# Optimization experiments

Hardware: AMD Instinct MI355X
Metric: run time of the kernel (lower is better)

Reference implementation:

```python
import jax, jax.numpy as jnp
import numpy as np

B, T, S = 4, 4096, 4096
D_MODEL = 512        # d_query = d_value_in = d_key_in
N_HEADS = 8
D_KEY = 512
D_VALUE = 512
N_OMEGA = 64
EPS = 1e-9
DK_H = D_KEY // N_HEADS      # 64
DV_H = D_VALUE // N_HEADS    # 64


def _glorot(key, shape):
    fan_in, fan_out = shape[-2], shape[-1]
    lim = np.sqrt(6.0 / (fan_in + fan_out))
    return jax.random.uniform(key, shape, jnp.float32, -lim, lim)


def _draw_omega(key, d_feature, n_omega):
    # n_omega == d_feature here -> single orthogonal block scaled by sqrt(d)
    g = jax.random.normal(key, (d_feature, d_feature), jnp.float32)
    q, _ = jnp.linalg.qr(g)
    q = q * jnp.sqrt(jnp.float32(d_feature))
    return q[:n_omega]


def setup_inputs() -> dict:
    key = jax.random.key(0)
    ks = jax.random.split(key, 7)
    return {
        "query": 0.5 * jax.random.normal(ks[0], (B, T, D_MODEL), jnp.float32),
        "value": 0.5 * jax.random.normal(ks[1], (B, S, D_MODEL), jnp.float32),
        "key": 0.5 * jax.random.normal(ks[2], (B, S, D_MODEL), jnp.float32),
        "wq": _glorot(ks[3], (N_HEADS, D_MODEL, DK_H)),
        "wv": _glorot(ks[4], (N_HEADS, D_MODEL, DV_H)),
        "wk": _glorot(ks[5], (N_HEADS, D_MODEL, DK_H)),
        "omega": _draw_omega(ks[6], DK_H, N_OMEGA),
    }


def _phi(x, omega):
    # x: (B,H,T,dk_h) -> (B,H,T,2*n_omega) FAVOR+ positive random features
    square_sum = 0.5 * jnp.sum(x * x, axis=-1, keepdims=True)
    xw = jnp.einsum('bhtk,mk->bhtm', x, omega)
    un = jnp.exp(jnp.concatenate([xw, -xw], axis=-1) - square_sum) + EPS
    return un / jnp.sqrt(jnp.float32(2.0 * N_OMEGA))


def reference(query, value, key, wq, wv, wk, omega):
    q = jnp.einsum('btf,hfk->bhtk', query, wq)   # (B,H,T,dk_h)
    v = jnp.einsum('bsd,hdk->bhsk', value, wv)   # (B,H,S,dv_h)
    k = jnp.einsum('bsf,hfk->bhsk', key, wk)     # (B,H,S,dk_h)
    qp = _phi(q, omega)                          # (B,H,T,2M)
    kp = _phi(k, omega)                          # (B,H,S,2M)
    v1 = jnp.concatenate([v, jnp.ones(v.shape[:-1] + (1,), v.dtype)], axis=-1)
    kv = jnp.einsum('bhsm,bhsd->bhmd', kp, v1)   # (B,H,2M,dv_h+1)
    qkv = jnp.einsum('bhtm,bhmd->bhtd', qp, kv)  # (B,H,T,dv_h+1)
    normalizer = qkv[..., -1:]
    out = qkv[..., :-1] / normalizer
    # faithful to original: plain reshape (B,H,T,dv_h) -> (B,T,D_VALUE), no transpose
    return jnp.reshape(out, (B, T, D_VALUE))
```

## Files before the change

### kernel.cpp

```cpp
#include <hip/hip_runtime.h>

typedef _Float16 half8 __attribute__((ext_vector_type(8)));
typedef _Float16 half4_t __attribute__((ext_vector_type(4)));
typedef short short8 __attribute__((ext_vector_type(8)));
typedef unsigned short u16x4 __attribute__((ext_vector_type(4)));
typedef float f32x4 __attribute__((ext_vector_type(4)));

#define NH 8

__device__ __forceinline__ unsigned short f2bf(float x) {
  union { float f; unsigned u; } v; v.f = x;
  unsigned r = v.u + 0x7FFFu + ((v.u >> 16) & 1u);
  return (unsigned short)(r >> 16);
}

#define DRAIN_BAR()                                  \
  asm volatile("s_waitcnt lgkmcnt(0)" ::: "memory"); \
  __builtin_amdgcn_s_barrier();                      \
  __builtin_amdgcn_sched_barrier(0)

__global__ __launch_bounds__(256) void k0_qk(
    const float* __restrict__ wq, const float* __restrict__ wk,
    const float* __restrict__ omega,
    _Float16* __restrict__ wxq, _Float16* __restrict__ wxk) {
  const int bid = blockIdx.x;
  const int arr = bid >> 7;
  const int h = (bid >> 4) & 7;
  const int ft = (bid >> 1) & 7;
  const int os = bid & 1;
  const int f = threadIdx.x & 63;
  const int w = threadIdx.x >> 6;
  const float* wsrc = (arr ? wk : wq) + ((size_t)h * 512 + ft * 64 + f) * 64;
  float wreg[64];
#pragma unroll
  for (int i = 0; i < 16; ++i) {
    float4 v = *(const float4*)(wsrc + i * 4);
    wreg[i * 4] = v.x; wreg[i * 4 + 1] = v.y; wreg[i * 4 + 2] = v.z; wreg[i * 4 + 3] = v.w;
  }
  _Float16* outp = arr ? wxk : wxq;
  const int k8 = f >> 3, e = f & 7;
#pragma unroll 1
  for (int oo = 0; oo < 8; ++oo) {
    const int o = w * 16 + os * 8 + oo;
    const float* om = omega + o * 64;
    float s = 0.f;
#pragma unroll
    for (int k = 0; k < 64; ++k) s = fmaf(wreg[k], om[k], s);
    outp[((((size_t)h * 8 + ft) * 8 + k8) * 64 + o) * 8 + e] = (_Float16)s;
  }
}

__global__ __launch_bounds__(256) void k0_v(
    const float* __restrict__ wv, _Float16* __restrict__ wvt) {
  int idx = blockIdx.x * 256 + threadIdx.x;
  int h = idx >> 15, o = (idx >> 9) & 63, f = idx & 511;
  float val = wv[((size_t)h * 512 + f) * 64 + o];
  wvt[((((size_t)h * 8 + (f >> 6)) * 8 + ((f >> 3) & 7)) * 64 + o) * 8 + (f & 7)] = (_Float16)val;
}

__global__ __launch_bounds__(512, 1) void fused_kv(
    const float* __restrict__ key, const float* __restrict__ value,
    const _Float16* __restrict__ wxk, const _Float16* __restrict__ wvt,
    float* __restrict__ kvpart) {
  __shared__ __align__(16) _Float16 A[2][128][72];
  __shared__ __align__(16) _Float16 W[2][2][4096];
  __shared__ __align__(16) unsigned short kpT[128][136];
  __shared__ __align__(16) unsigned short vT[64][136];
  const int bid = blockIdx.x;
  const int hp = bid >> 6;
  const int b = (bid >> 4) & 3;
  const int sc = bid & 15;
  const int s0 = sc * 256;
  const int tid = threadIdx.x;
  const int w = tid >> 6;
  const int lane = tid & 63;
  const int g = lane >> 4, c = lane & 15;
  const int hh = w >> 2;
  const int rq = w & 3;
  const int xr = lane >> 4;
  const int xc = (lane & 15) * 4;

  const _Float16* wkb0 = wxk + (size_t)(hp * 2) * 32768;
  const _Float16* wkb1 = wkb0 + 32768;
  const _Float16* wvb0 = wvt + (size_t)(hp * 2) * 32768;
  const _Float16* wvb1 = wvb0 + 32768;

  short8 bones;
#pragma unroll
  for (int i = 0; i < 8; ++i) bones[i] = (c == 0) ? (short)0x3F80 : (short)0;

  f32x4 acc_kv[2][5];
#pragma unroll
  for (int h2 = 0; h2 < 2; ++h2)
#pragma unroll
    for (int j = 0; j < 5; ++j) acc_kv[h2][j] = (f32x4){0.f, 0.f, 0.f, 0.f};

  u16x4 kps[2][4], kms[2][4], vs_[2][4];

  float4 xv[4];
  half8 wr0, wr1;

#pragma unroll 1
  for (int p = 0; p < 4; ++p) {
    const float* xb = ((p & 1) ? value : key) +
                      (size_t)(b * 4096 + s0 + (p >> 1) * 128 + w * 16 + xr) * 512 + xc;
    const _Float16* wb0 = (p & 1) ? wvb0 : wkb0;
    const _Float16* wb1 = (p & 1) ? wvb1 : wkb1;

#pragma unroll
    for (int i = 0; i < 4; ++i) xv[i] = *(const float4*)(xb + i * 2048);
    wr0 = *(const half8*)(wb0 + tid * 8);
    wr1 = *(const half8*)(wb1 + tid * 8);
#pragma unroll
    for (int i = 0; i < 4; ++i) {
      float vv[4] = {xv[i].x, xv[i].y, xv[i].z, xv[i].w};
      half4_t hv;
#pragma unroll
      for (int j2 = 0; j2 < 4; ++j2) hv[j2] = (_Float16)vv[j2];
      *(half4_t*)&A[0][w * 16 + i * 4 + xr][xc] = hv;
    }
    *(half8*)&W[0][0][tid * 8] = wr0;
    *(half8*)&W[0][1][tid * 8] = wr1;
#pragma unroll
    for (int i = 0; i < 4; ++i) xv[i] = *(const float4*)(xb + 64 + i * 2048);
    wr0 = *(const half8*)(wb0 + 4096 + tid * 8);
    wr1 = *(const half8*)(wb1 + 4096 + tid * 8);
    DRAIN_BAR();

    f32x4 accp[2][4];
#pragma unroll
    for (int mf = 0; mf < 2; ++mf)
#pragma unroll
      for (int j = 0; j < 4; ++j) accp[mf][j] = (f32x4){0.f, 0.f, 0.f, 0.f};

#pragma unroll 1
    for (int kc = 0; kc < 8; ++kc) {
      const int cur = kc & 1;
      if (kc < 7) {
        const int nxt = cur ^ 1;
#pragma unroll
        for (int i = 0; i < 4; ++i) {
          float vv[4] = {xv[i].x, xv[i].y, xv[i].z, xv[i].w};
          half4_t hv;
#pragma unroll
          for (int j2 = 0; j2 < 4; ++j2) hv[j2] = (_Float16)vv[j2];
          *(half4_t*)&A[nxt][w * 16 + i * 4 + xr][xc] = hv;
        }
        *(half8*)&W[nxt][0][tid * 8] = wr0;
        *(half8*)&W[nxt][1][tid * 8] = wr1;
        if (kc < 6) {
#pragma unroll
          for (int i = 0; i < 4; ++i)
            xv[i] = *(const float4*)(xb + (kc + 2) * 64 + i * 2048);
          wr0 = *(const half8*)(wb0 + (kc + 2) * 4096 + tid * 8);
          wr1 = *(const half8*)(wb1 + (kc + 2) * 4096 + tid * 8);
        }
      }
#pragma unroll
      for (int ks = 0; ks < 2; ++ks) {
        half8 af0 = *(const half8*)&A[cur][rq * 32 + c][ks * 32 + g * 8];
        half8 af1 = *(const half8*)&A[cur][rq * 32 + 16 + c][ks * 32 + g * 8];
#pragma unroll
        for (int nf = 0; nf < 4; ++nf) {
          half8 wf = *(const half8*)&W[cur][hh][((ks * 4 + g) * 64 + nf * 16 + c) * 8];
          accp[0][nf] = __builtin_amdgcn_mfma_f32_16x16x32_f16(af0, wf, accp[0][nf], 0, 0, 0);
          accp[1][nf] = __builtin_amdgcn_mfma_f32_16x16x32_f16(af1, wf, accp[1][nf], 0, 0, 0);
        }
      }
      DRAIN_BAR();
    }

    if ((p & 1) == 0) {
#pragma unroll
      for (int mf = 0; mf < 2; ++mf) {
        float ss_[4];
#pragma unroll
        for (int j = 0; j < 4; ++j) {
          float s = 0.f;
#pragma unroll
          for (int nf = 0; nf < 4; ++nf) { float q = accp[mf][nf][j]; s = fmaf(q, q, s); }
          s += __shfl_xor(s, 1); s += __shfl_xor(s, 2);
          s += __shfl_xor(s, 4); s += __shfl_xor(s, 8);
          ss_[j] = s * 0.0078125f;
        }
#pragma unroll
        for (int nf = 0; nf < 4; ++nf) {
          u16x4 kp_p, kp_m;
#pragma unroll
          for (int j = 0; j < 4; ++j) {
            float v = accp[mf][nf][j];
            kp_p[j] = f2bf(__expf(v - ss_[j]) + 1e-9f);
            kp_m[j] = f2bf(__expf(-v - ss_[j]) + 1e-9f);
          }
          kps[mf][nf] = kp_p;
          kms[mf][nf] = kp_m;
        }
      }
    } else {
#pragma unroll
      for (int mf = 0; mf < 2; ++mf)
#pragma unroll
        for (int nf = 0; nf < 4; ++nf) {
          u16x4 vv;
#pragma unroll
          for (int j = 0; j < 4; ++j) vv[j] = f2bf(accp[mf][nf][j]);
          vs_[mf][nf] = vv;
        }
#pragma unroll
      for (int h2 = 0; h2 < 2; ++h2) {
        if (hh == h2) {
#pragma unroll
          for (int mf = 0; mf < 2; ++mf)
#pragma unroll
            for (int nf = 0; nf < 4; ++nf) {
              const int m = nf * 16 + c;
              const int sl = rq * 32 + mf * 16 + g * 4;
              *(u16x4*)&kpT[m][sl] = kps[mf][nf];
              *(u16x4*)&kpT[64 + m][sl] = kms[mf][nf];
              *(u16x4*)&vT[m][sl] = vs_[mf][nf];
            }
        }
        DRAIN_BAR();
#pragma unroll
        for (int ks = 0; ks < 4; ++ks) {
          short8 a = *(const short8*)&kpT[w * 16 + c][ks * 32 + g * 8];
#pragma unroll
          for (int nf = 0; nf < 4; ++nf) {
            short8 bb = *(const short8*)&vT[nf * 16 + c][ks * 32 + g * 8];
            acc_kv[h2][nf] = __builtin_amdgcn_mfma_f32_16x16x32_bf16(a, bb, acc_kv[h2][nf], 0, 0, 0);
          }
          acc_kv[h2][4] = __builtin_amdgcn_mfma_f32_16x16x32_bf16(a, bones, acc_kv[h2][4], 0, 0, 0);
        }
        __builtin_amdgcn_s_barrier();
      }
    }
  }

#pragma unroll
  for (int h2 = 0; h2 < 2; ++h2) {
    float* pbase = kvpart + ((size_t)sc * 32 + b * 8 + hp * 2 + h2) * 10240;
#pragma unroll
    for (int nf = 0; nf < 5; ++nf)
#pragma unroll
      for (int j = 0; j < 4; ++j)
        pbase[(w * 16 + g * 4 + j) * 80 + nf * 16 + c] = acc_kv[h2][nf][j];
  }
}

__global__ __launch_bounds__(128) void k3a_denom(
    const float* __restrict__ kvpart, float* __restrict__ invbuf,
    float* __restrict__ lsc) {
  const int bh = blockIdx.x;
  const int m = threadIdx.x;
  const float* base = kvpart + (size_t)bh * 10240 + m * 80 + 64;
  float s = 0.f;
#pragma unroll
  for (int kk = 0; kk < 16; ++kk) s += base[(size_t)kk * 327680];
  invbuf[bh * 128 + m] = 1.0f / s;
  lsc[bh * 128 + m] = __logf(s);
}

__global__ __launch_bounds__(256) void k3b_reduce(
    const float* __restrict__ kvpart, const float* __restrict__ invbuf,
    _Float16* __restrict__ kvnt) {
  const int bh = blockIdx.x;
  const int e0 = blockIdx.y * 1024 + threadIdx.x * 4;
  const int m = e0 / 80;
  const int d0 = e0 - m * 80;
  const float* base = kvpart + (size_t)bh * 10240 + e0;
  f32x4 s = (f32x4){0.f, 0.f, 0.f, 0.f};
#pragma unroll
  for (int kk = 0; kk < 16; ++kk) {
    f32x4 v = *(const f32x4*)(base + (size_t)kk * 327680);
    s += v;
  }
  const float inv = invbuf[bh * 128 + m];
  const int mst = ((m & 63) << 1) | (m >> 6);
  _Float16* outb = kvnt + (size_t)bh * 10240 + mst;
#pragma unroll
  for (int j = 0; j < 4; ++j) {
    const int d = d0 + j;
    float val;
    if (d < 64) val = s[j] * inv;
    else if (d == 64) val = 1.0f;
    else val = 0.f;
    outb[d * 128] = (_Float16)val;
  }
}

__global__ __launch_bounds__(256, 2) void fused_qo(
    const float* __restrict__ query, const _Float16* __restrict__ wxq,
    const _Float16* __restrict__ kvnt, const float* __restrict__ lsc,
    float* __restrict__ out) {
  __shared__ __align__(16) _Float16 A[64][264];
  __shared__ __align__(16) _Float16 W[2][4096];
  __shared__ __align__(16) _Float16 qpT[64][136];
  const int bid = blockIdx.x;
  const int hh2 = bid >> 8;
  const int b = (bid >> 6) & 3;
  const int tt = bid & 63;
  const int t0 = tt * 64;
  const int tid = threadIdx.x;
  const int w = tid >> 6;
  const int lane = tid & 63;
  const int g = lane >> 4, c = lane & 15;
  const int arow = tid >> 2;
  const int ac4 = (tid & 3) * 16;

  const float* xrow = query + (size_t)(b * 4096 + t0 + arow) * 512 + ac4;
  const _Float16* wbase = wxq;

  f32x4 accp[4][4];
#pragma unroll
  for (int h = 0; h < 4; ++h)
#pragma unroll
    for (int j = 0; j < 4; ++j) accp[h][j] = (f32x4){0.f, 0.f, 0.f, 0.f};

  float4 xv[4];
  half8 wr0, wr1;

#pragma unroll
  for (int i = 0; i < 4; ++i) xv[i] = *(const float4*)(xrow + i * 64);

#pragma unroll
  for (int kh = 0; kh < 2; ++kh) {
#pragma unroll
    for (int i = 0; i < 4; ++i) {
      float4 v0 = xv[i];
      half4_t hv;
      hv[0] = (_Float16)v0.x; hv[1] = (_Float16)v0.y;
      hv[2] = (_Float16)v0.z; hv[3] = (_Float16)v0.w;
      *(half4_t*)&A[arow][ac4 + i * 4] = hv;
    }
#pragma unroll
    for (int i = 0; i < 4; ++i) {
      float4 v0 = xv[i];
      half4_t hv;
      hv[0] = (_Float16)v0.x; hv[1] = (_Float16)v0.y;
      hv[2] = (_Float16)v0.z; hv[3] = (_Float16)v0.w;
      *(half4_t*)&A[arow][ac4 + i * 64] = hv;
    }
#pragma unroll
    for (int i = 0; i < 4; ++i) {
#pragma unroll
      for (int q2 = 1; q2 < 4; ++q2) {
        float4 v = *(const float4*)(xrow + kh * 256 + i * 64 + q2 * 4);
        half4_t hv;
        hv[0] = (_Float16)v.x; hv[1] = (_Float16)v.y;
        hv[2] = (_Float16)v.z; hv[3] = (_Float16)v.w;
        *(half4_t*)&A[arow][ac4 + i * 64 + q2 * 4] = hv;
      }
    }
    {
      const _Float16* wsl0 = wbase + ((size_t)(hh2 * 4 + 0) * 8 + kh * 4 + 0) * 4096;
      wr0 = *(const half8*)(wsl0 + tid * 8);
      wr1 = *(const half8*)(wsl0 + 2048 + tid * 8);
      *(half8*)&W[0][tid * 8] = wr0;
      *(half8*)&W[0][2048 + tid * 8] = wr1;
      const _Float16* wsl1 = wbase + ((size_t)(hh2 * 4 + 0) * 8 + kh * 4 + 1) * 4096;
      wr0 = *(const half8*)(wsl1 + tid * 8);
      wr1 = *(const half8*)(wsl1 + 2048 + tid * 8);
    }
    DRAIN_BAR();
    if (kh == 0) {
#pragma unroll
      for (int i = 0; i < 4; ++i) xv[i] = *(const float4*)(xrow + 256 + i * 64);
    }

#pragma unroll
    for (int h = 0; h < 4; ++h) {
#pragma unroll
      for (int kc = 0; kc < 4; ++kc) {
        const int s = h * 4 + kc;
        const int cur = s & 1;
        if (s < 15) {
          *(half8*)&W[cur ^ 1][tid * 8] = wr0;
          *(half8*)&W[cur ^ 1][2048 + tid * 8] = wr1;
        }
        if (s < 14) {
          const int sn = s + 2;
          const _Float16* wsl = wbase +
              ((size_t)(hh2 * 4 + (sn >> 2)) * 8 + kh * 4 + (sn & 3)) * 4096;
          wr0 = *(const half8*)(wsl + tid * 8);
          wr1 = *(const half8*)(wsl + 2048 + tid * 8);
        }
#pragma unroll
        for (int ks = 0; ks < 2; ++ks) {
          half8 a = *(const half8*)&A[w * 16 + c][kc * 64 + ks * 32 + g * 8];
#pragma unroll
          for (int nf = 0; nf < 4; ++nf) {
            half8 wf = *(const half8*)&W[cur][((ks * 4 + g) * 64 + nf * 16 + c) * 8];
            accp[h][nf] = __builtin_amdgcn_mfma_f32_16x16x32_f16(a, wf, accp[h][nf], 0, 0, 0);
          }
        }
        DRAIN_BAR();
      }
    }
  }

#pragma unroll
  for (int h = 0; h < 4; ++h) {
    const int bh = b * NH + hh2 * 4 + h;
    float Lp[4], Lm[4];
#pragma unroll
    for (int nf = 0; nf < 4; ++nf) {
      Lp[nf] = lsc[bh * 128 + nf * 16 + c];
      Lm[nf] = lsc[bh * 128 + 64 + nf * 16 + c];
    }
    float ss_[4], cm_[4];
#pragma unroll
    for (int j = 0; j < 4; ++j) {
      float s = 0.f;
#pragma unroll
      for (int nf = 0; nf < 4; ++nf) { float q = accp[h][nf][j]; s = fmaf(q, q, s); }
      s += __shfl_xor(s, 1); s += __shfl_xor(s, 2);
      s += __shfl_xor(s, 4); s += __shfl_xor(s, 8);
      ss_[j] = s * 0.0078125f;
    }
#pragma unroll
    for (int j = 0; j < 4; ++j) {
      float m0 = -1e30f;
#pragma unroll
      for (int nf = 0; nf < 4; ++nf) {
        float v = accp[h][nf][j];
        m0 = fmaxf(m0, fmaxf(v - ss_[j] + Lp[nf], -v - ss_[j] + Lm[nf]));
        m0 = fmaxf(m0, fmaxf(Lp[nf], Lm[nf]) - 20.723265f);
      }
      m0 = fmaxf(m0, __shfl_xor(m0, 1)); m0 = fmaxf(m0, __shfl_xor(m0, 2));
      m0 = fmaxf(m0, __shfl_xor(m0, 4)); m0 = fmaxf(m0, __shfl_xor(m0, 8));
      cm_[j] = m0;
    }
#pragma unroll
    for (int nf = 0; nf < 4; ++nf) {
      const int m = nf * 16 + c;
#pragma unroll
      for (int j = 0; j < 4; ++j) {
        float v = accp[h][nf][j];
        _Float16 pp = (_Float16)(__expf(v - ss_[j] + Lp[nf] - cm_[j]) +
                                 1e-9f * __expf(Lp[nf] - cm_[j]));
        _Float16 pm = (_Float16)(__expf(-v - ss_[j] + Lm[nf] - cm_[j]) +
                                 1e-9f * __expf(Lm[nf] - cm_[j]));
        union { unsigned u; _Float16 hh_[2]; } pk;
        pk.hh_[0] = pp; pk.hh_[1] = pm;
        *(unsigned*)&qpT[w * 16 + g * 4 + j][2 * m] = pk.u;
      }
    }
    DRAIN_BAR();

    f32x4 acco[5];
#pragma unroll
    for (int j = 0; j < 5; ++j) acco[j] = (f32x4){0.f, 0.f, 0.f, 0.f};
    const _Float16* kvb = kvnt + (size_t)bh * 10240;
#pragma unroll
    for (int ks = 0; ks < 4; ++ks) {
      half8 a = *(const half8*)&qpT[w * 16 + c][ks * 32 + g * 8];
#pragma unroll
      for (int nf = 0; nf < 5; ++nf) {
        half8 bb = *(const half8*)(kvb + (size_t)(nf * 16 + c) * 128 + ks * 32 + g * 8);
        acco[nf] = __builtin_amdgcn_mfma_f32_16x16x32_f16(a, bb, acco[nf], 0, 0, 0);
      }
    }
    const int tb = t0 + w * 16 + g * 4;
#pragma unroll
    for (int j = 0; j < 4; ++j) {
      float nrm = __shfl(acco[4][j], (lane & 48));
      float invn = 1.0f / nrm;
#pragma unroll
      for (int nf = 0; nf < 4; ++nf) {
        out[((size_t)bh * 4096 + tb + j) * 64 + nf * 16 + c] = acco[nf][j] * invn;
      }
    }
    DRAIN_BAR();
  }
}

extern "C" void kernel_launch(void* const* d_in, const int* in_sizes, int n_in,
                              void* d_out, int out_size, void* d_ws, size_t ws_size,
                              hipStream_t stream) {
  const float* query = (const float*)d_in[0];
  const float* value = (const float*)d_in[1];
  const float* key   = (const float*)d_in[2];
  const float* wq    = (const float*)d_in[3];
  const float* wv    = (const float*)d_in[4];
  const float* wk    = (const float*)d_in[5];
  const float* omega = (const float*)d_in[6];
  float* out = (float*)d_out;
  char* ws = (char*)d_ws;

  _Float16* wxq  = (_Float16*)(ws);
  _Float16* wxk  = (_Float16*)(ws + 524288);
  _Float16* wvt  = (_Float16*)(ws + 1048576);
  float* kvpart  = (float*)(ws + 1572864);
  _Float16* kvnt = (_Float16*)(ws + 22544384);
  float* lsc     = (float*)(ws + 23199744);
  float* invbuf  = (float*)(ws + 23216128);

  k0_qk<<<256, 256, 0, stream>>>(wq, wk, omega, wxq, wxk);
  k0_v<<<1024, 256, 0, stream>>>(wv, wvt);
  fused_kv<<<256, 512, 0, stream>>>(key, value, wxk, wvt, kvpart);
  k3a_denom<<<32, 128, 0, stream>>>(kvpart, invbuf, lsc);
  k3b_reduce<<<dim3(32, 10), 256, 0, stream>>>(kvpart, invbuf, kvnt);
  fused_qo<<<512, 256, 0, stream>>>(query, wxq, kvnt, lsc, out);
}
```

Measured before the change: 111.3 us.

## Stream fused_qo weights via direct global-to-LDS loads with 4-deep ring buffer

Rewrites the query projection loop in fused_qo so weight tiles go straight from global memory into a 4-slot LDS ring with global_load_lds, issued three stages ahead and gated by vmcnt waits. The register round-trip disappears and each step now needs only one barrier instead of a drain. The A tile shrinks to 128-wide chunks that are reused as the qp buffer, which lowers LDS usage enough to raise occupancy to 3 blocks per SM. The cost is more barrier stages (4 K-chunks instead of 2) and fragile hand-tuned vmcnt counts.

After: 113.9 us. 1.02x slower.

```diff
diff --git a/kernel.cpp b/kernel.cpp
--- a/kernel.cpp
+++ b/kernel.cpp
@@ -18,6 +18,13 @@
   asm volatile("s_waitcnt lgkmcnt(0)" ::: "memory"); \
   __builtin_amdgcn_s_barrier();                      \
   __builtin_amdgcn_sched_barrier(0)
+
+#define WAITVM(N) asm volatile("s_waitcnt vmcnt(" #N ")" ::: "memory")
+
+#define GLOAD_LDS16(g, l)                                             \
+  __builtin_amdgcn_global_load_lds(                                   \
+      (const __attribute__((address_space(1))) unsigned int*)(g),     \
+      (__attribute__((address_space(3))) unsigned int*)(l), 16, 0, 0)
 
 __global__ __launch_bounds__(256) void k0_qk(
     const float* __restrict__ wq, const float* __restrict__ wk,
@@ -288,13 +295,12 @@
   }
 }
 
-__global__ __launch_bounds__(256, 2) void fused_qo(
+__global__ __launch_bounds__(256, 3) void fused_qo(
     const float* __restrict__ query, const _Float16* __restrict__ wxq,
     const _Float16* __restrict__ kvnt, const float* __restrict__ lsc,
     float* __restrict__ out) {
-  __shared__ __align__(16) _Float16 A[64][264];
-  __shared__ __align__(16) _Float16 W[2][4096];
-  __shared__ __align__(16) _Float16 qpT[64][136];
+  __shared__ __align__(16) _Float16 A_[64][136];
+  __shared__ __align__(16) _Float16 W4[4][4096];
   const int bid = blockIdx.x;
   const int hh2 = bid >> 8;
   const int b = (bid >> 6) & 3;
@@ -305,10 +311,10 @@
   const int lane = tid & 63;
   const int g = lane >> 4, c = lane & 15;
   const int arow = tid >> 2;
-  const int ac4 = (tid & 3) * 16;
-
-  const float* xrow = query + (size_t)(b * 4096 + t0 + arow) * 512 + ac4;
-  const _Float16* wbase = wxq;
+  const int acb = (tid & 3) * 32;
+
+  const float* xq = query + (size_t)(b * 4096 + t0 + arow) * 512 + acb;
+  const char* wbase = (const char*)wxq;
 
   f32x4 accp[4][4];
 #pragma unroll
@@ -316,87 +322,70 @@
 #pragma unroll
     for (int j = 0; j < 4; ++j) accp[h][j] = (f32x4){0.f, 0.f, 0.f, 0.f};
 
-  float4 xv[4];
-  half8 wr0, wr1;
-
-#pragma unroll
-  for (int i = 0; i < 4; ++i) xv[i] = *(const float4*)(xrow + i * 64);
-
-#pragma unroll
-  for (int kh = 0; kh < 2; ++kh) {
-#pragma unroll
-    for (int i = 0; i < 4; ++i) {
-      float4 v0 = xv[i];
-      half4_t hv;
-      hv[0] = (_Float16)v0.x; hv[1] = (_Float16)v0.y;
-      hv[2] = (_Float16)v0.z; hv[3] = (_Float16)v0.w;
-      *(half4_t*)&A[arow][ac4 + i * 4] = hv;
-    }
-#pragma unroll
-    for (int i = 0; i < 4; ++i) {
-      float4 v0 = xv[i];
-      half4_t hv;
-      hv[0] = (_Float16)v0.x; hv[1] = (_Float16)v0.y;
-      hv[2] = (_Float16)v0.z; hv[3] = (_Float16)v0.w;
-      *(half4_t*)&A[arow][ac4 + i * 64] = hv;
-    }
-#pragma unroll
-    for (int i = 0; i < 4; ++i) {
-#pragma unroll
-      for (int q2 = 1; q2 < 4; ++q2) {
-        float4 v = *(const float4*)(xrow + kh * 256 + i * 64 + q2 * 4);
-        half4_t hv;
-        hv[0] = (_Float16)v.x; hv[1] = (_Float16)v.y;
-        hv[2] = (_Float16)v.z; hv[3] = (_Float16)v.w;
-        *(half4_t*)&A[arow][ac4 + i * 64 + q2 * 4] = hv;
-      }
-    }
-    {
-      const _Float16* wsl0 = wbase + ((size_t)(hh2 * 4 + 0) * 8 + kh * 4 + 0) * 4096;
-      wr0 = *(const half8*)(wsl0 + tid * 8);
-      wr1 = *(const half8*)(wsl0 + 2048 + tid * 8);
-      *(half8*)&W[0][tid * 8] = wr0;
-      *(half8*)&W[0][2048 + tid * 8] = wr1;
-      const _Float16* wsl1 = wbase + ((size_t)(hh2 * 4 + 0) * 8 + kh * 4 + 1) * 4096;
-      wr0 = *(const half8*)(wsl1 + tid * 8);
-      wr1 = *(const half8*)(wsl1 + 2048 + tid * 8);
+  float4 xv[8];
+
+#define ISSUE_W(S)                                                              \
+  do {                                                                          \
+    const int kq_ = (S) >> 3, loc_ = (S) & 7, h_ = loc_ >> 1, kc2_ = loc_ & 1;  \
+    const size_t woff = (((size_t)(hh2 * 4 + h_) * 8 + kq_ * 2 + kc2_) * 4096) * 2; \
+    const char* gb = wbase + woff + (w * 2) * 1024 + lane * 16;                 \
+    char* lb = (char*)&W4[(S) & 3][0] + (w * 2) * 1024;                         \
+    GLOAD_LDS16(gb, lb);                                                        \
+    GLOAD_LDS16(gb + 1024, lb + 1024);                                          \
+  } while (0)
+
+#pragma unroll
+  for (int i = 0; i < 8; ++i) xv[i] = *(const float4*)(xq + i * 4);
+  ISSUE_W(0);
+  ISSUE_W(1);
+  ISSUE_W(2);
+
+#pragma unroll
+  for (int kq = 0; kq < 4; ++kq) {
+    if (kq > 0) { DRAIN_BAR(); }
+#pragma unroll
+    for (int i = 0; i < 8; i += 2) {
+      half8 hv;
+      hv[0] = (_Float16)xv[i].x;     hv[1] = (_Float16)xv[i].y;
+      hv[2] = (_Float16)xv[i].z;     hv[3] = (_Float16)xv[i].w;
+      hv[4] = (_Float16)xv[i + 1].x; hv[5] = (_Float16)xv[i + 1].y;
+      hv[6] = (_Float16)xv[i + 1].z; hv[7] = (_Float16)xv[i + 1].w;
+      *(half8*)&A_[arow][acb + i * 4] = hv;
     }
     DRAIN_BAR();
-    if (kh == 0) {
-#pragma unroll
-      for (int i = 0; i < 4; ++i) xv[i] = *(const float4*)(xrow + 256 + i * 64);
-    }
-
-#pragma unroll
-    for (int h = 0; h < 4; ++h) {
-#pragma unroll
-      for (int kc = 0; kc < 4; ++kc) {
-        const int s = h * 4 + kc;
-        const int cur = s & 1;
-        if (s < 15) {
-          *(half8*)&W[cur ^ 1][tid * 8] = wr0;
-          *(half8*)&W[cur ^ 1][2048 + tid * 8] = wr1;
-        }
-        if (s < 14) {
-          const int sn = s + 2;
-          const _Float16* wsl = wbase +
-              ((size_t)(hh2 * 4 + (sn >> 2)) * 8 + kh * 4 + (sn & 3)) * 4096;
-          wr0 = *(const half8*)(wsl + tid * 8);
-          wr1 = *(const half8*)(wsl + 2048 + tid * 8);
-        }
-#pragma unroll
-        for (int ks = 0; ks < 2; ++ks) {
-          half8 a = *(const half8*)&A[w * 16 + c][kc * 64 + ks * 32 + g * 8];
-#pragma unroll
-          for (int nf = 0; nf < 4; ++nf) {
-            half8 wf = *(const half8*)&W[cur][((ks * 4 + g) * 64 + nf * 16 + c) * 8];
-            accp[h][nf] = __builtin_amdgcn_mfma_f32_16x16x32_f16(a, wf, accp[h][nf], 0, 0, 0);
-          }
-        }
-        DRAIN_BAR();
-      }
-    }
-  }
+
+#pragma unroll
+    for (int loc = 0; loc < 8; ++loc) {
+      const int S = kq * 8 + loc;
+      if (S == 31)      { WAITVM(0); }
+      else if (S == 30) { WAITVM(2); }
+      else if (loc >= 6){ WAITVM(12); }
+      else              { WAITVM(4); }
+      __builtin_amdgcn_s_barrier();
+      __builtin_amdgcn_sched_barrier(0);
+      if (S + 3 < 32) ISSUE_W(S + 3);
+      if (loc == 5 && kq < 3) {
+#pragma unroll
+        for (int i = 0; i < 8; ++i)
+          xv[i] = *(const float4*)(xq + (kq + 1) * 128 + i * 4);
+      }
+      const int h = loc >> 1;
+      const int kc2 = loc & 1;
+      const int buf = S & 3;
+#pragma unroll
+      for (int ks = 0; ks < 2; ++ks) {
+        half8 a = *(const half8*)&A_[w * 16 + c][kc2 * 64 + ks * 32 + g * 8];
+#pragma unroll
+        for (int nf = 0; nf < 4; ++nf) {
+          half8 wf = *(const half8*)&W4[buf][((ks * 4 + g) * 64 + nf * 16 + c) * 8];
+          accp[h][nf] = __builtin_amdgcn_mfma_f32_16x16x32_f16(a, wf, accp[h][nf], 0, 0, 0);
+        }
+      }
+    }
+  }
+#undef ISSUE_W
+
+  DRAIN_BAR();
 
 #pragma unroll
   for (int h = 0; h < 4; ++h) {
@@ -442,7 +431,7 @@
                                  1e-9f * __expf(Lm[nf] - cm_[j]));
         union { unsigned u; _Float16 hh_[2]; } pk;
         pk.hh_[0] = pp; pk.hh_[1] = pm;
-        *(unsigned*)&qpT[w * 16 + g * 4 + j][2 * m] = pk.u;
+        *(unsigned*)&A_[w * 16 + g * 4 + j][2 * m] = pk.u;
       }
     }
     DRAIN_BAR();
@@ -453,7 +442,7 @@
     const _Float16* kvb = kvnt + (size_t)bh * 10240;
 #pragma unroll
     for (int ks = 0; ks < 4; ++ks) {
-      half8 a = *(const half8*)&qpT[w * 16 + c][ks * 32 + g * 8];
+      half8 a = *(const half8*)&A_[w * 16 + c][ks * 32 + g * 8];
 #pragma unroll
       for (int nf = 0; nf < 5; ++nf) {
         half8 bb = *(const half8*)(kvb + (size_t)(nf * 16 + c) * 128 + ks * 32 + g * 8);
```
